# Optimization experiments

Measured on AMD Instinct MI355X. Metric: run time of the kernel, lower is better.

The kernel has to match this reference:

```python
import jax, jax.numpy as jnp
import numpy as np

EPS = 1e-12


def _cosine_cost_volume(ref, tgt, D):
    """PSMNet-style shifted cosine-correlation cost volume, num_groups=1.
    ref, tgt: [B, C, Hf, Wf] quarter-res features. Returns [B, 1, D, Hf, Wf];
    positions w < d are 0 (zero-padded target -> zero cosine)."""
    B, C, Hf, Wf = ref.shape
    rn = ref * jax.lax.rsqrt(jnp.sum(ref * ref, axis=1, keepdims=True) + EPS)
    tn = tgt * jax.lax.rsqrt(jnp.sum(tgt * tgt, axis=1, keepdims=True) + EPS)
    pad = jnp.pad(tn, ((0, 0), (0, 0), (0, 0), (D - 1, 0)))  # left zero-pad

    def one_disp(d):
        t = jax.lax.dynamic_slice_in_dim(pad, D - 1 - d, Wf, axis=3)
        return jnp.sum(rn * t, axis=1)  # [B, Hf, Wf]

    vol = jax.vmap(one_disp)(jnp.arange(D))  # [D, B, Hf, Wf]
    return jnp.transpose(vol, (1, 0, 2, 3))[:, None]  # [B, 1, D, Hf, Wf]


def setup_inputs() -> dict:
    key = jax.random.key(0)
    k1, k2 = jax.random.split(key)
    B, C, Hf, Wf = 1, 32, 96, 192  # quarter-res ViT features (out_feats=32)
    left_fea = jax.random.normal(k1, (B, C, Hf, Wf), dtype=jnp.float32)
    right_fea = jax.random.normal(k2, (B, C, Hf, Wf), dtype=jnp.float32)
    return {"left_fea": left_fea, "right_fea": right_fea, "H": 384, "W": 768, "maxdisp": 192}


def reference(left_fea, right_fea, H, W, maxdisp):
    B = left_fea.shape[0]
    # training-branch cost volume (W//4 disparity levels, not detached in source)
    cost_init = _cosine_cost_volume(left_fea, right_fea, W // 4)
    # inference path: maxdisp//4 levels, trilinear upsample to [maxdisp, H, W]
    cost = _cosine_cost_volume(left_fea, right_fea, maxdisp // 4)
    cost = jax.lax.stop_gradient(cost)
    cost_up = jax.image.resize(cost, (B, 1, maxdisp, H, W), method="trilinear")
    pred = jnp.argmax(cost_up, axis=2)  # [B, 1, H, W]
    pred = jnp.maximum(pred, 1).astype(jnp.float32)  # pred[pred<1]=1
    return cost_init, pred
```

## Files before the change

kernel.cpp:

```cpp
#include <hip/hip_runtime.h>
#include <math.h>

#define HF 96
#define WF 192
#define CC 32
#define NPIX (HF*WF)
#define DFULL 192
#define DQ 48
#define HO 384
#define WO 768

__global__ __launch_bounds__(256) void knorm(const float* __restrict__ L,
                                             const float* __restrict__ R,
                                             float* __restrict__ inv) {
    int pid = blockIdx.x * 256 + threadIdx.x;
    if (pid >= 2 * NPIX) return;
    const float* p = (pid < NPIX) ? L : R;
    int off = (pid < NPIX) ? pid : pid - NPIX;
    float s = 0.0f;
    #pragma unroll
    for (int c = 0; c < CC; ++c) {
        float v = p[c * NPIX + off];
        s = fmaf(v, v, s);
    }
    inv[pid] = 1.0f / sqrtf(s + 1e-12f);
}

__global__ __launch_bounds__(192) void kcost(const float* __restrict__ L,
                                             const float* __restrict__ R,
                                             const float* __restrict__ inv,
                                             float* __restrict__ out) {
    __shared__ __align__(16) float rs[WF * 36];
    const int h  = blockIdx.x;
    const int d0 = blockIdx.y * 48;
    const int tid = threadIdx.x;

    for (int i = tid; i < WF * CC; i += 192) {
        int c = i / WF;
        int w = i - c * WF;
        rs[w * 36 + c] = R[c * NPIX + h * WF + w] * inv[NPIX + h * WF + w];
    }

    const int w = tid;
    float lreg[CC];
    {
        float invl = inv[h * WF + w];
        #pragma unroll
        for (int c = 0; c < CC; ++c)
            lreg[c] = L[c * NPIX + h * WF + w] * invl;
    }
    __syncthreads();

    for (int dd = 0; dd < 48; ++dd) {
        int d = d0 + dd;
        int wp = w - d;
        float acc = 0.0f;
        if (wp >= 0) {
            const float* r = &rs[wp * 36];
            #pragma unroll
            for (int c = 0; c < CC; ++c)
                acc = fmaf(lreg[c], r[c], acc);
        }
        out[(d * HF + h) * WF + w] = acc;
    }
}

__global__ __launch_bounds__(256) void kpred(const float* __restrict__ cost,
                                             float* __restrict__ pred) {
    int pid = blockIdx.x * 256 + threadIdx.x;
    if (pid >= HO * WO) return;
    int w = pid % WO;
    int h = pid / WO;

    float sh = (float)(2 * h - 3) * 0.125f;
    float fh = sh - floorf(sh);
    int h0 = (int)floorf(sh);
    int h1 = h0 + 1;
    if (h0 < 0)      { h0 = 0;      h1 = 0;      fh = 0.0f; }
    if (h1 > HF - 1) { h1 = HF - 1;              fh = 0.0f; }

    float sw = (float)(2 * w - 3) * 0.125f;
    float fw = sw - floorf(sw);
    int w0 = (int)floorf(sw);
    int w1 = w0 + 1;
    if (w0 < 0)      { w0 = 0;      w1 = 0;      fw = 0.0f; }
    if (w1 > WF - 1) { w1 = WF - 1;              fw = 0.0f; }

    const float wh0 = 1.0f - fh, wh1 = fh;
    const float ww0 = 1.0f - fw, ww1 = fw;

    const int i00 = h0 * WF + w0;
    const int i10 = h1 * WF + w0;
    const int i01 = h0 * WF + w1;
    const int i11 = h1 * WF + w1;

    auto bilin = [&](int k) -> float {
        const float* s = cost + k * NPIX;
        float v00 = s[i00], v10 = s[i10], v01 = s[i01], v11 = s[i11];
        float a0 = fmaf(wh1, v10, wh0 * v00);
        float a1 = fmaf(wh1, v11, wh0 * v01);
        return fmaf(ww1, a1, ww0 * a0);
    };

    float bprev = bilin(0);
    float best = bprev;
    int bidx = 0;

    for (int k = 1; k < DQ; ++k) {
        float b = bilin(k);
        #pragma unroll
        for (int t = 0; t < 4; ++t) {
            float f = 0.125f + 0.25f * (float)t;
            float v = fmaf(f, b, (1.0f - f) * bprev);
            if (v > best) { best = v; bidx = 4 * k - 2 + t; }
        }
        bprev = b;
    }
    if (bprev > best) { best = bprev; bidx = 190; }

    pred[pid] = (float)(bidx < 1 ? 1 : bidx);
}

extern "C" void kernel_launch(void* const* d_in, const int* in_sizes, int n_in,
                              void* d_out, int out_size, void* d_ws, size_t ws_size,
                              hipStream_t stream) {
    const float* L = (const float*)d_in[0];
    const float* R = (const float*)d_in[1];
    float* out = (float*)d_out;
    float* pred = out + DFULL * NPIX;
    float* inv = (float*)d_ws;

    knorm<<<(2 * NPIX + 255) / 256, 256, 0, stream>>>(L, R, inv);
    kcost<<<dim3(HF, 4), 192, 0, stream>>>(L, R, inv, out);
    kpred<<<(HO * WO + 255) / 256, 256, 0, stream>>>(out, pred);
}
```

Baseline: 105.1 us.

## Fuse norm computation into cost kernel and interleave disparities across blocks

Removes the separate normalization kernel and computes the inverse L2 norms of the left and right features inside the cost-volume kernel, dropping one launch and the workspace round-trip. Shared memory switches from a padded [w][c] layout to a [c][w] layout so threads read consecutive words. Disparities are now interleaved across the four y-blocks (d = 4*dd + y) instead of contiguous chunks, which balances the amount of skipped w<d work across blocks. The cost is that each of the four y-blocks recomputes the norms redundantly.

```diff
diff --git a/kernel.cpp b/kernel.cpp
--- a/kernel.cpp
+++ b/kernel.cpp
@@ -10,56 +10,53 @@
 #define HO 384
 #define WO 768
 
-__global__ __launch_bounds__(256) void knorm(const float* __restrict__ L,
-                                             const float* __restrict__ R,
-                                             float* __restrict__ inv) {
-    int pid = blockIdx.x * 256 + threadIdx.x;
-    if (pid >= 2 * NPIX) return;
-    const float* p = (pid < NPIX) ? L : R;
-    int off = (pid < NPIX) ? pid : pid - NPIX;
-    float s = 0.0f;
-    #pragma unroll
-    for (int c = 0; c < CC; ++c) {
-        float v = p[c * NPIX + off];
-        s = fmaf(v, v, s);
-    }
-    inv[pid] = 1.0f / sqrtf(s + 1e-12f);
-}
-
 __global__ __launch_bounds__(192) void kcost(const float* __restrict__ L,
                                              const float* __restrict__ R,
-                                             const float* __restrict__ inv,
                                              float* __restrict__ out) {
-    __shared__ __align__(16) float rs[WF * 36];
-    const int h  = blockIdx.x;
-    const int d0 = blockIdx.y * 48;
-    const int tid = threadIdx.x;
+    __shared__ float rs[CC * WF];
+    const int h = blockIdx.x;
+    const int y = blockIdx.y;
+    const int w = threadIdx.x;
 
-    for (int i = tid; i < WF * CC; i += 192) {
-        int c = i / WF;
-        int w = i - c * WF;
-        rs[w * 36 + c] = R[c * NPIX + h * WF + w] * inv[NPIX + h * WF + w];
+    {
+        float rreg[CC];
+        float s = 0.0f;
+        #pragma unroll
+        for (int c = 0; c < CC; ++c) {
+            float v = R[c * NPIX + h * WF + w];
+            rreg[c] = v;
+            s = fmaf(v, v, s);
+        }
+        float rinv = 1.0f / sqrtf(s + 1e-12f);
+        #pragma unroll
+        for (int c = 0; c < CC; ++c)
+            rs[c * WF + w] = rreg[c] * rinv;
     }
 
-    const int w = tid;
     float lreg[CC];
     {
-        float invl = inv[h * WF + w];
+        float s = 0.0f;
         #pragma unroll
-        for (int c = 0; c < CC; ++c)
-            lreg[c] = L[c * NPIX + h * WF + w] * invl;
+        for (int c = 0; c < CC; ++c) {
+            float v = L[c * NPIX + h * WF + w];
+            lreg[c] = v;
+            s = fmaf(v, v, s);
+        }
+        float linv = 1.0f / sqrtf(s + 1e-12f);
+        #pragma unroll
+        for (int c = 0; c < CC; ++c) lreg[c] *= linv;
     }
+
     __syncthreads();
 
     for (int dd = 0; dd < 48; ++dd) {
-        int d = d0 + dd;
+        int d = 4 * dd + y;
         int wp = w - d;
         float acc = 0.0f;
         if (wp >= 0) {
-            const float* r = &rs[wp * 36];
             #pragma unroll
             for (int c = 0; c < CC; ++c)
-                acc = fmaf(lreg[c], r[c], acc);
+                acc = fmaf(lreg[c], rs[c * WF + wp], acc);
         }
         out[(d * HF + h) * WF + w] = acc;
     }
@@ -76,15 +73,15 @@
     float fh = sh - floorf(sh);
     int h0 = (int)floorf(sh);
     int h1 = h0 + 1;
-    if (h0 < 0)      { h0 = 0;      h1 = 0;      fh = 0.0f; }
-    if (h1 > HF - 1) { h1 = HF - 1;              fh = 0.0f; }
+    if (h0 < 0)      { h0 = 0; h1 = 0; fh = 0.0f; }
+    if (h1 > HF - 1) { h1 = HF - 1;    fh = 0.0f; }
 
     float sw = (float)(2 * w - 3) * 0.125f;
     float fw = sw - floorf(sw);
     int w0 = (int)floorf(sw);
     int w1 = w0 + 1;
-    if (w0 < 0)      { w0 = 0;      w1 = 0;      fw = 0.0f; }
-    if (w1 > WF - 1) { w1 = WF - 1;              fw = 0.0f; }
+    if (w0 < 0)      { w0 = 0; w1 = 0; fw = 0.0f; }
+    if (w1 > WF - 1) { w1 = WF - 1;    fw = 0.0f; }
 
     const float wh0 = 1.0f - fh, wh1 = fh;
     const float ww0 = 1.0f - fw, ww1 = fw;
@@ -128,9 +125,7 @@
     const float* R = (const float*)d_in[1];
     float* out = (float*)d_out;
     float* pred = out + DFULL * NPIX;
-    float* inv = (float*)d_ws;
 
-    knorm<<<(2 * NPIX + 255) / 256, 256, 0, stream>>>(L, R, inv);
-    kcost<<<dim3(HF, 4), 192, 0, stream>>>(L, R, inv, out);
+    kcost<<<dim3(HF, 4), 192, 0, stream>>>(L, R, out);
     kpred<<<(HO * WO + 255) / 256, 256, 0, stream>>>(out, pred);
 }
```

Result: faster. 102.6 us (-2.4%).
